# Optimization experiments

Hardware: AMD Instinct MI355X
Metric: run time of the kernel (lower is better)

## Reference

```python
import jax, jax.numpy as jnp
import numpy as np

N, IC, H, OC, E = 50000, 128, 128, 64, 800000
EPS = 1e-5


def _sage(x, src, dst, wl, wr, b):
    # PyG SAGEConv (mean aggr): out = lin_l(mean_j x_j) + lin_r(x)
    msg = x[src]                                    # [E, d] gather
    s = jax.ops.segment_sum(msg, dst, num_segments=N)
    cnt = jax.ops.segment_sum(jnp.ones((src.shape[0],), x.dtype), dst, num_segments=N)
    mean = s / jnp.clip(cnt, 1.0)[:, None]
    return mean @ wl.T + b + x @ wr.T


def _bn_relu(x, g, be):
    # training-mode BatchNorm1d over node axis (biased var), then ReLU
    m = jnp.mean(x, axis=0)
    v = jnp.mean((x - m) ** 2, axis=0)
    return jax.nn.relu((x - m) * jax.lax.rsqrt(v + EPS) * g + be)


def setup_inputs() -> dict:
    key = jax.random.key(0)
    ks = jax.random.split(key, 16)
    d = {
        "x": jax.random.normal(ks[0], (N, IC), jnp.float32),
        "ei": jax.random.randint(ks[1], (2, E), 0, N, jnp.int32),
        # SAGEConv 1..3: lin_l (with bias) on aggregated, lin_r (no bias) on root
        "w1l": jax.random.normal(ks[2], (H, IC), jnp.float32) / np.sqrt(IC),
        "w1r": jax.random.normal(ks[3], (H, IC), jnp.float32) / np.sqrt(IC),
        "b1c": jnp.zeros((H,), jnp.float32),
        "w2l": jax.random.normal(ks[4], (H, H), jnp.float32) / np.sqrt(H),
        "w2r": jax.random.normal(ks[5], (H, H), jnp.float32) / np.sqrt(H),
        "b2c": jnp.zeros((H,), jnp.float32),
        "w3l": jax.random.normal(ks[6], (H, H), jnp.float32) / np.sqrt(H),
        "w3r": jax.random.normal(ks[7], (H, H), jnp.float32) / np.sqrt(H),
        "b3c": jnp.zeros((H,), jnp.float32),
        # BatchNorm affine params
        "g1": jnp.ones((H,), jnp.float32), "be1": jnp.zeros((H,), jnp.float32),
        "g2": jnp.ones((H,), jnp.float32), "be2": jnp.zeros((H,), jnp.float32),
        "g3": jnp.ones((H,), jnp.float32), "be3": jnp.zeros((H,), jnp.float32),
        # head Linear
        "wh": jax.random.normal(ks[8], (OC, H), jnp.float32) / np.sqrt(H),
        "bh": jnp.zeros((OC,), jnp.float32),
    }
    return d


def reference(x, ei, w1l, w1r, b1c, w2l, w2r, b2c, w3l, w3r, b3c,
              g1, be1, g2, be2, g3, be3, wh, bh):
    src, dst = ei[0], ei[1]
    h = _bn_relu(_sage(x, src, dst, w1l, w1r, b1c), g1, be1)
    # dropout omitted (deterministic reference / eval semantics)
    h = _bn_relu(_sage(h, src, dst, w2l, w2r, b2c), g2, be2)
    h = _bn_relu(_sage(h, src, dst, w3l, w3r, b3c), g3, be3)
    return h @ wh.T + bh
```

## Files before the change

kernel.cpp:

```cpp
#include <hip/hip_runtime.h>

static constexpr int FC = 128;

typedef __attribute__((ext_vector_type(8))) __bf16 bf16x8;
typedef __attribute__((ext_vector_type(4))) float f32x4;

__device__ __forceinline__ unsigned short f2bf(float f) {
  unsigned u = __float_as_uint(f);
  unsigned r = (u + 0x7FFF + ((u >> 16) & 1)) >> 16;
  return (unsigned short)r;
}
__device__ __forceinline__ float bf2f(unsigned short h) {
  return __uint_as_float((unsigned)h << 16);
}
__device__ __forceinline__ unsigned pk_i8x4(int q0, int q1, int q2, int q3) {
  return (unsigned)(q0 & 0xff) | ((unsigned)(q1 & 0xff) << 8) |
         ((unsigned)(q2 & 0xff) << 16) | ((unsigned)(q3 & 0xff) << 24);
}

__global__ __launch_bounds__(256) void zero_kernel(int* __restrict__ deg,
                                                   float* __restrict__ stats, int n) {
  int i = blockIdx.x * 256 + threadIdx.x;
  if (i < n) deg[i] = 0;
  if (i < 768) stats[i] = 0.f;
}

__global__ __launch_bounds__(256) void convert_kernel(
    const float* __restrict__ x, const float* __restrict__ w1l, const float* __restrict__ w1r,
    const float* __restrict__ w2l, const float* __restrict__ w2r,
    const float* __restrict__ w3l, const float* __restrict__ w3r,
    const float* __restrict__ wh,
    unsigned short* __restrict__ x_bf, unsigned* __restrict__ xi8,
    float* __restrict__ xsc,
    unsigned short* __restrict__ wc1,
    unsigned short* __restrict__ wc2, unsigned short* __restrict__ wc3,
    unsigned short* __restrict__ whb, int n, int nxq) {
  int b = blockIdx.x;
  int t = threadIdx.x;
  if (b < nxq) {
    int row = b * 8 + (t >> 5);
    int lane = t & 31;
    if (row >= n) return;
    float4 a = *reinterpret_cast<const float4*>(x + (size_t)row * FC + lane * 4);
    ushort4 o = {f2bf(a.x), f2bf(a.y), f2bf(a.z), f2bf(a.w)};
    *reinterpret_cast<ushort4*>(x_bf + (size_t)row * FC + lane * 4) = o;
    float m = fmaxf(fmaxf(fabsf(a.x), fabsf(a.y)), fmaxf(fabsf(a.z), fabsf(a.w)));
    m = fmaxf(m, __shfl_xor(m, 1));
    m = fmaxf(m, __shfl_xor(m, 2));
    m = fmaxf(m, __shfl_xor(m, 4));
    m = fmaxf(m, __shfl_xor(m, 8));
    m = fmaxf(m, __shfl_xor(m, 16));
    float inv = 127.0f / fmaxf(m, 1e-30f);
    int q0 = (int)rintf(a.x * inv), q1 = (int)rintf(a.y * inv);
    int q2 = (int)rintf(a.z * inv), q3 = (int)rintf(a.w * inv);
    xi8[(size_t)row * 32 + lane] = pk_i8x4(q0, q1, q2, q3);
    if (lane == 0) xsc[row] = m * (1.0f / 127.0f);
    return;
  }
  int r = b - nxq;
  if (r < 48) {
    int layer = r >> 4;
    const float* wl = layer == 0 ? w1l : (layer == 1 ? w2l : w3l);
    const float* wr = layer == 0 ? w1r : (layer == 1 ? w2r : w3r);
    unsigned short* out = layer == 0 ? wc1 : (layer == 1 ? wc2 : wc3);
    int i = (r & 15) * 256 + t;
    int row = i >> 5;
    int k8 = (i & 31) * 8;
    const float* src = (k8 < 128) ? (wl + (size_t)row * 128 + k8)
                                  : (wr + (size_t)row * 128 + (k8 - 128));
    float4 a = *reinterpret_cast<const float4*>(src);
    float4 c = *reinterpret_cast<const float4*>(src + 4);
    ushort4 o0 = {f2bf(a.x), f2bf(a.y), f2bf(a.z), f2bf(a.w)};
    ushort4 o1 = {f2bf(c.x), f2bf(c.y), f2bf(c.z), f2bf(c.w)};
    unsigned short* q = out + (size_t)row * 256 + k8;
    *reinterpret_cast<ushort4*>(q) = o0;
    *reinterpret_cast<ushort4*>(q + 4) = o1;
  } else {
    int i = (r - 48) * 256 + t;
    const float* p = wh + (size_t)i * 8;
    float4 a = *reinterpret_cast<const float4*>(p);
    float4 c = *reinterpret_cast<const float4*>(p + 4);
    ushort4 o0 = {f2bf(a.x), f2bf(a.y), f2bf(a.z), f2bf(a.w)};
    ushort4 o1 = {f2bf(c.x), f2bf(c.y), f2bf(c.z), f2bf(c.w)};
    unsigned short* q = whb + (size_t)i * 8;
    *reinterpret_cast<ushort4*>(q) = o0;
    *reinterpret_cast<ushort4*>(q + 4) = o1;
  }
}

__global__ void count_kernel(const int* __restrict__ dst, int* __restrict__ deg,
                             int* __restrict__ rank, int e) {
  int i = blockIdx.x * blockDim.x + threadIdx.x;
  if (i < e) rank[i] = atomicAdd(&deg[dst[i]], 1);
}

__global__ __launch_bounds__(256) void scan1_kernel(const int* __restrict__ deg,
                                                    int* __restrict__ bsum, int n) {
  int i = blockIdx.x * 256 + threadIdx.x;
  int v = (i < n) ? deg[i] : 0;
  __shared__ int ls[256];
  ls[threadIdx.x] = v;
  __syncthreads();
  for (int d = 128; d > 0; d >>= 1) {
    if (threadIdx.x < (unsigned)d) ls[threadIdx.x] += ls[threadIdx.x + d];
    __syncthreads();
  }
  if (threadIdx.x == 0) bsum[blockIdx.x] = ls[0];
}

__global__ __launch_bounds__(256) void scan23_kernel(const int* __restrict__ deg,
                                                     const int* __restrict__ bsum,
                                                     int* __restrict__ off, int n, int nb) {
  __shared__ int bls[256];
  __shared__ int ls[256];
  int t = threadIdx.x;
  int bv = (t < nb) ? bsum[t] : 0;
  bls[t] = bv;
  __syncthreads();
  for (int d = 1; d < 256; d <<= 1) {
    int u = (t >= d) ? bls[t - d] : 0;
    __syncthreads();
    bls[t] += u;
    __syncthreads();
  }
  int i = blockIdx.x * 256 + t;
  int v = (i < n) ? deg[i] : 0;
  ls[t] = v;
  __syncthreads();
  for (int d = 1; d < 256; d <<= 1) {
    int u = (t >= d) ? ls[t - d] : 0;
    __syncthreads();
    ls[t] += u;
    __syncthreads();
  }
  int base = blockIdx.x ? bls[blockIdx.x - 1] : 0;
  if (i < n) off[i] = base + ls[t] - v;
  if (blockIdx.x == 0 && t == 0) off[n] = bls[nb - 1];
}

__global__ void fill_kernel(const int* __restrict__ src, const int* __restrict__ dst,
                            const int* __restrict__ rank, const int* __restrict__ off,
                            int* __restrict__ csr, int e) {
  int i = blockIdx.x * blockDim.x + threadIdx.x;
  if (i < e) csr[off[dst[i]] + rank[i]] = src[i];
}

template <bool BNIN>
__global__ __launch_bounds__(256) void aggregate_kernel(const unsigned* __restrict__ xi8,
                                                        const float* __restrict__ xsc,
                                                        const int* __restrict__ off,
                                                        const int* __restrict__ csr,
                                                        unsigned short* __restrict__ agg,
                                                        const float* __restrict__ stats,
                                                        const float* __restrict__ g,
                                                        const float* __restrict__ be,
                                                        float invn, int n) {
  int hw = (int)((blockIdx.x * blockDim.x + threadIdx.x) >> 5);
  int lane = threadIdx.x & 31;
  if (hw >= n) return;

  float sc0 = 1.f, sc1 = 1.f, sc2 = 1.f, sc3 = 1.f;
  float sh0 = 0.f, sh1 = 0.f, sh2 = 0.f, sh3 = 0.f;
  if (BNIN) {
    int c0 = lane * 4;
    float4 s  = *reinterpret_cast<const float4*>(stats + c0);
    float4 s2 = *reinterpret_cast<const float4*>(stats + 128 + c0);
    float4 gv = *reinterpret_cast<const float4*>(g + c0);
    float4 bv = *reinterpret_cast<const float4*>(be + c0);
    float m0 = s.x * invn, m1 = s.y * invn, m2 = s.z * invn, m3 = s.w * invn;
    sc0 = gv.x * rsqrtf(fmaxf(s2.x * invn - m0 * m0, 0.f) + 1e-5f);
    sc1 = gv.y * rsqrtf(fmaxf(s2.y * invn - m1 * m1, 0.f) + 1e-5f);
    sc2 = gv.z * rsqrtf(fmaxf(s2.z * invn - m2 * m2, 0.f) + 1e-5f);
    sc3 = gv.w * rsqrtf(fmaxf(s2.w * invn - m3 * m3, 0.f) + 1e-5f);
    sh0 = bv.x - m0 * sc0; sh1 = bv.y - m1 * sc1;
    sh2 = bv.z - m2 * sc2; sh3 = bv.w - m3 * sc3;
  }

  int s0 = off[hw], s1 = off[hw + 1];
  float a0 = 0.f, a1 = 0.f, a2 = 0.f, a3 = 0.f;

#define ACCV(u, sv)                                               \
  {                                                               \
    float q0 = (float)(((int)(u) << 24) >> 24);                   \
    float q1 = (float)(((int)(u) << 16) >> 24);                   \
    float q2 = (float)(((int)(u) << 8) >> 24);                    \
    float q3 = (float)((int)(u) >> 24);                           \
    if (BNIN) {                                                   \
      a0 += fmaxf(fmaf(q0, (sv) * sc0, sh0), 0.f);                \
      a1 += fmaxf(fmaf(q1, (sv) * sc1, sh1), 0.f);                \
      a2 += fmaxf(fmaf(q2, (sv) * sc2, sh2), 0.f);                \
      a3 += fmaxf(fmaf(q3, (sv) * sc3, sh3), 0.f);                \
    } else {                                                      \
      a0 = fmaf(q0, (sv), a0);                                    \
      a1 = fmaf(q1, (sv), a1);                                    \
      a2 = fmaf(q2, (sv), a2);                                    \
      a3 = fmaf(q3, (sv), a3);                                    \
    }                                                             \
  }

  int j = s0;
  for (; j + 8 <= s1; j += 8) {
    int i0 = csr[j],     i1 = csr[j + 1], i2 = csr[j + 2], i3 = csr[j + 3];
    int i4 = csr[j + 4], i5 = csr[j + 5], i6 = csr[j + 6], i7 = csr[j + 7];
    unsigned u0 = xi8[(size_t)i0 * 32 + lane];
    unsigned u1 = xi8[(size_t)i1 * 32 + lane];
    unsigned u2 = xi8[(size_t)i2 * 32 + lane];
    unsigned u3 = xi8[(size_t)i3 * 32 + lane];
    unsigned u4 = xi8[(size_t)i4 * 32 + lane];
    unsigned u5 = xi8[(size_t)i5 * 32 + lane];
    unsigned u6 = xi8[(size_t)i6 * 32 + lane];
    unsigned u7 = xi8[(size_t)i7 * 32 + lane];
    float sv0 = xsc[i0], sv1 = xsc[i1], sv2 = xsc[i2], sv3 = xsc[i3];
    float sv4 = xsc[i4], sv5 = xsc[i5], sv6 = xsc[i6], sv7 = xsc[i7];
    ACCV(u0, sv0) ACCV(u1, sv1) ACCV(u2, sv2) ACCV(u3, sv3)
    ACCV(u4, sv4) ACCV(u5, sv5) ACCV(u6, sv6) ACCV(u7, sv7)
  }
  for (; j < s1; j++) {
    int i0 = csr[j];
    unsigned u0 = xi8[(size_t)i0 * 32 + lane];
    float sv0 = xsc[i0];
    ACCV(u0, sv0)
  }
#undef ACCV

  int d = s1 - s0;
  float inv = 1.0f / (float)(d > 0 ? d : 1);
  ushort4 o = {f2bf(a0 * inv), f2bf(a1 * inv), f2bf(a2 * inv), f2bf(a3 * inv)};
  *reinterpret_cast<ushort4*>(agg + (size_t)hw * FC + lane * 4) = o;
}

template <int NCOLS, int KTOT, bool DUAL, bool OUT_BF, bool STATS, bool BNIN, bool OUT_I8>
__global__ __launch_bounds__(256) void gemm_kernel(const unsigned short* __restrict__ A1,
                                                   const unsigned short* __restrict__ A2,
                                                   const unsigned short* __restrict__ W,
                                                   const float* __restrict__ bias,
                                                   void* __restrict__ Cout,
                                                   unsigned char* __restrict__ h8,
                                                   float* __restrict__ hsc,
                                                   float* __restrict__ statsOut,
                                                   const float* __restrict__ statsIn,
                                                   const float* __restrict__ g,
                                                   const float* __restrict__ be,
                                                   float invn, int nrows) {
  constexpr int NKT = KTOT / 32;
  constexpr int NCF = NCOLS / 16;
  constexpr int RB = KTOT * 2;
  constexpr int WBYTES = NCOLS * KTOT * 2;
  __shared__ __align__(16) unsigned char Wl[WBYTES];
  __shared__ float scv[128], shv[128];

  int t = threadIdx.x;

  {
    constexpr int CH = WBYTES / 16 / 256;
#pragma unroll
    for (int c = 0; c < CH; c++) {
      int byte = (c * 256 + t) * 16;
      int row = byte / RB;
      int cb = byte % RB;
      float4 v = *reinterpret_cast<const float4*>(reinterpret_cast<const char*>(W) + byte);
      *reinterpret_cast<float4*>(Wl + row * RB + (cb ^ ((row & 7) << 4))) = v;
    }
  }

  if (BNIN && t < 128) {
    float mean = statsIn[t] * invn;
    float var = fmaxf(statsIn[128 + t] * invn - mean * mean, 0.f);
    float s = g[t] * rsqrtf(var + 1e-5f);
    scv[t] = s;
    shv[t] = be[t] - mean * s;
  }

  int w = t >> 6;
  int l = t & 63;
  int lm = l & 15;
  int hi = l >> 4;
  int lk = hi * 8;
  int row = blockIdx.x * 64 + w * 16 + lm;
  int rclamp = min(row, nrows - 1);

  bf16x8 a[NKT];
#pragma unroll
  for (int kt = 0; kt < NKT; kt++) {
    const unsigned short* Ap;
    int kk;
    if (!DUAL || kt < NKT / 2) { Ap = A1; kk = kt * 32; }
    else                       { Ap = A2; kk = (kt - NKT / 2) * 32; }
    a[kt] = *reinterpret_cast<const bf16x8*>(Ap + (size_t)rclamp * 128 + kk + lk);
  }

  f32x4 acc[NCF];
#pragma unroll
  for (int cf = 0; cf < NCF; cf++) acc[cf] = {0.f, 0.f, 0.f, 0.f};

  __syncthreads();

  if (BNIN) {
#pragma unroll
    for (int kt = 0; kt < NKT; kt++) {
      if (!DUAL || kt >= NKT / 2) {
        int ch0 = (DUAL ? (kt - NKT / 2) : kt) * 32 + lk;
#pragma unroll
        for (int j = 0; j < 8; j++) {
          float v = (float)a[kt][j];
          v = fmaxf(fmaf(v, scv[ch0 + j], shv[ch0 + j]), 0.f);
          a[kt][j] = (__bf16)v;
        }
      }
    }
  }

#pragma unroll
  for (int kt = 0; kt < NKT; kt++) {
#pragma unroll
    for (int cf = 0; cf < NCF; cf++) {
      int r = cf * 16 + lm;
      int cb = kt * 64 + hi * 16;
      bf16x8 b = *reinterpret_cast<const bf16x8*>(Wl + r * RB + (cb ^ ((r & 7) << 4)));
      acc[cf] = __builtin_amdgcn_mfma_f32_16x16x32_bf16(a[kt], b, acc[cf], 0, 0, 0);
    }
  }

#pragma unroll
  for (int cf = 0; cf < NCF; cf++) {
    float bs = bias[cf * 16 + lm];
#pragma unroll
    for (int r = 0; r < 4; r++) acc[cf][r] += bs;
  }

  float qinv[4], qs[4];
  if (OUT_I8) {
#pragma unroll
    for (int r = 0; r < 4; r++) {
      float m = 0.f;
#pragma unroll
      for (int cf = 0; cf < NCF; cf++) m = fmaxf(m, fabsf(acc[cf][r]));
      m = fmaxf(m, __shfl_xor(m, 1));
      m = fmaxf(m, __shfl_xor(m, 2));
      m = fmaxf(m, __shfl_xor(m, 4));
      m = fmaxf(m, __shfl_xor(m, 8));
      qinv[r] = 127.0f / fmaxf(m, 1e-30f);
      qs[r] = m * (1.0f / 127.0f);
    }
  }

  __shared__ float wsum[4][NCOLS];
  __shared__ float wsq[4][NCOLS];

  int orow0 = blockIdx.x * 64 + w * 16 + hi * 4;
#pragma unroll
  for (int cf = 0; cf < NCF; cf++) {
    int col = cf * 16 + lm;
    float s = 0.f, s2 = 0.f;
#pragma unroll
    for (int r = 0; r < 4; r++) {
      int orow = orow0 + r;
      bool ok = orow < nrows;
      float v = acc[cf][r];
      if (ok) {
        if (OUT_BF)
          ((unsigned short*)Cout)[(size_t)orow * NCOLS + col] = f2bf(v);
        else
          ((float*)Cout)[(size_t)orow * NCOLS + col] = v;
        if (OUT_I8)
          h8[(size_t)orow * NCOLS + col] = (unsigned char)((int)rintf(v * qinv[r]) & 0xff);
      }
      if (STATS) {
        float vv = ok ? v : 0.f;
        s += vv; s2 += vv * vv;
      }
    }
    if (STATS) {
      s  += __shfl_xor(s, 16);  s  += __shfl_xor(s, 32);
      s2 += __shfl_xor(s2, 16); s2 += __shfl_xor(s2, 32);
      if (l < 16) { wsum[w][col] = s; wsq[w][col] = s2; }
    }
  }
  if (OUT_I8 && lm == 0) {
#pragma unroll
    for (int r = 0; r < 4; r++) {
      int orow = orow0 + r;
      if (orow < nrows) hsc[orow] = qs[r];
    }
  }
  if (STATS) {
    __syncthreads();
    if (t < NCOLS) {
      atomicAdd(&statsOut[t], wsum[0][t] + wsum[1][t] + wsum[2][t] + wsum[3][t]);
    } else if (t < 2 * NCOLS) {
      int c = t - NCOLS;
      atomicAdd(&statsOut[t], wsq[0][c] + wsq[1][c] + wsq[2][c] + wsq[3][c]);
    }
  }
}

extern "C" void kernel_launch(void* const* d_in, const int* in_sizes, int n_in,
                              void* d_out, int out_size, void* d_ws, size_t ws_size,
                              hipStream_t stream) {
  const float* x   = (const float*)d_in[0];
  const int*   ei  = (const int*)d_in[1];
  const float* w1l = (const float*)d_in[2];
  const float* w1r = (const float*)d_in[3];
  const float* b1c = (const float*)d_in[4];
  const float* w2l = (const float*)d_in[5];
  const float* w2r = (const float*)d_in[6];
  const float* b2c = (const float*)d_in[7];
  const float* w3l = (const float*)d_in[8];
  const float* w3r = (const float*)d_in[9];
  const float* b3c = (const float*)d_in[10];
  const float* g1  = (const float*)d_in[11];
  const float* be1 = (const float*)d_in[12];
  const float* g2  = (const float*)d_in[13];
  const float* be2 = (const float*)d_in[14];
  const float* g3  = (const float*)d_in[15];
  const float* be3 = (const float*)d_in[16];
  const float* wh  = (const float*)d_in[17];
  const float* bh  = (const float*)d_in[18];

  int n = in_sizes[0] / FC;
  int e = in_sizes[1] / 2;
  const int* srcI = ei;
  const int* dstI = ei + e;

  char* p = (char*)d_ws;
  auto take = [&](size_t bytes) {
    char* q = p;
    p += (bytes + 255) & ~(size_t)255;
    return q;
  };
  int nb = (n + 255) / 256;
  int* deg  = (int*)take((size_t)n * 4);
  int* off  = (int*)take((size_t)(n + 1) * 4);
  int* bsum = (int*)take((size_t)nb * 4);
  int* rank = (int*)take((size_t)e * 4);
  int* csr  = (int*)take((size_t)e * 4);
  unsigned short* x_bf = (unsigned short*)take((size_t)n * FC * 2);
  unsigned short* agg  = (unsigned short*)take((size_t)n * FC * 2);
  unsigned short* h1   = (unsigned short*)take((size_t)n * FC * 2);
  unsigned short* h2   = (unsigned short*)take((size_t)n * FC * 2);
  unsigned char*  ai8  = (unsigned char*)take((size_t)n * FC);
  float*          asc  = (float*)take((size_t)n * 4);
  unsigned short* wc1  = (unsigned short*)take(128 * 256 * 2);
  unsigned short* wc2  = (unsigned short*)take(128 * 256 * 2);
  unsigned short* wc3  = (unsigned short*)take(128 * 256 * 2);
  unsigned short* whb  = (unsigned short*)take(64 * 128 * 2);
  float* stats = (float*)take(3 * 256 * 4);

  float invn = 1.0f / (float)n;
  int nxq = (n + 7) / 8;

  zero_kernel<<<nb, 256, 0, stream>>>(deg, stats, n);
  convert_kernel<<<nxq + 52, 256, 0, stream>>>(x, w1l, w1r, w2l, w2r, w3l, w3r, wh,
                                               x_bf, (unsigned*)ai8, asc,
                                               wc1, wc2, wc3, whb, n, nxq);

  count_kernel<<<(e + 255) / 256, 256, 0, stream>>>(dstI, deg, rank, e);
  scan1_kernel<<<nb, 256, 0, stream>>>(deg, bsum, n);
  scan23_kernel<<<nb, 256, 0, stream>>>(deg, bsum, off, n, nb);
  fill_kernel<<<(e + 255) / 256, 256, 0, stream>>>(srcI, dstI, rank, off, csr, e);

  int gb = (n + 63) / 64;
  int ab = (n + 7) / 8;

  aggregate_kernel<false><<<ab, 256, 0, stream>>>((const unsigned*)ai8, asc, off, csr, agg,
                                                  nullptr, nullptr, nullptr, invn, n);
  gemm_kernel<128, 256, true, true, true, false, true><<<gb, 256, 0, stream>>>(
      agg, x_bf, wc1, b1c, h1, ai8, asc, stats, nullptr, nullptr, nullptr, invn, n);

  aggregate_kernel<true><<<ab, 256, 0, stream>>>((const unsigned*)ai8, asc, off, csr, agg,
                                                 stats, g1, be1, invn, n);
  gemm_kernel<128, 256, true, true, true, true, true><<<gb, 256, 0, stream>>>(
      agg, h1, wc2, b2c, h2, ai8, asc, stats + 256, stats, g1, be1, invn, n);

  aggregate_kernel<true><<<ab, 256, 0, stream>>>((const unsigned*)ai8, asc, off, csr, agg,
                                                 stats + 256, g2, be2, invn, n);
  gemm_kernel<128, 256, true, true, true, true, false><<<gb, 256, 0, stream>>>(
      agg, h2, wc3, b3c, h1, nullptr, nullptr, stats + 512, stats + 256, g2, be2, invn, n);

  gemm_kernel<64, 128, false, false, false, true, false><<<gb, 256, 0, stream>>>(
      h1, nullptr, whb, bh, d_out, nullptr, nullptr, nullptr, stats + 512, g3, be3, invn, n);
}
```

Baseline: 261.7 us.

## Split int8 feature table into two column halves and aggregate each half separately

The int8 quantized node features are stored as two separate 64-column tables, and each aggregation is split into two launches, one per half, using 16 lanes per node. Each half table is 3.2 MB instead of 6.4 MB, so the random neighbor gathers should hit in cache more often. CSR index reads become nontemporal loads. The cost is that the CSR indices and scales are read twice and there are extra kernel launches.

Measured after the change: 313.1 us. +19.7%, slower.

```diff
diff --git a/kernel.cpp b/kernel.cpp
--- a/kernel.cpp
+++ b/kernel.cpp
@@ -30,7 +30,7 @@
     const float* __restrict__ w2l, const float* __restrict__ w2r,
     const float* __restrict__ w3l, const float* __restrict__ w3r,
     const float* __restrict__ wh,
-    unsigned short* __restrict__ x_bf, unsigned* __restrict__ xi8,
+    unsigned short* __restrict__ x_bf, unsigned* __restrict__ ta, unsigned* __restrict__ tb,
     float* __restrict__ xsc,
     unsigned short* __restrict__ wc1,
     unsigned short* __restrict__ wc2, unsigned short* __restrict__ wc3,
@@ -53,7 +53,9 @@
     float inv = 127.0f / fmaxf(m, 1e-30f);
     int q0 = (int)rintf(a.x * inv), q1 = (int)rintf(a.y * inv);
     int q2 = (int)rintf(a.z * inv), q3 = (int)rintf(a.w * inv);
-    xi8[(size_t)row * 32 + lane] = pk_i8x4(q0, q1, q2, q3);
+    unsigned u = pk_i8x4(q0, q1, q2, q3);
+    if (lane < 16) ta[(size_t)row * 16 + lane] = u;
+    else           tb[(size_t)row * 16 + (lane - 16)] = u;
     if (lane == 0) xsc[row] = m * (1.0f / 127.0f);
     return;
   }
@@ -145,8 +147,8 @@
   if (i < e) csr[off[dst[i]] + rank[i]] = src[i];
 }
 
-template <bool BNIN>
-__global__ __launch_bounds__(256) void aggregate_kernel(const unsigned* __restrict__ xi8,
+template <int HALF, bool BNIN>
+__global__ __launch_bounds__(256) void aggregate_kernel(const unsigned* __restrict__ tab,
                                                         const float* __restrict__ xsc,
                                                         const int* __restrict__ off,
                                                         const int* __restrict__ csr,
@@ -155,14 +157,14 @@
                                                         const float* __restrict__ g,
                                                         const float* __restrict__ be,
                                                         float invn, int n) {
-  int hw = (int)((blockIdx.x * blockDim.x + threadIdx.x) >> 5);
-  int lane = threadIdx.x & 31;
-  if (hw >= n) return;
+  int node = (int)((blockIdx.x * blockDim.x + threadIdx.x) >> 4);
+  int lane = threadIdx.x & 15;
+  if (node >= n) return;
 
   float sc0 = 1.f, sc1 = 1.f, sc2 = 1.f, sc3 = 1.f;
   float sh0 = 0.f, sh1 = 0.f, sh2 = 0.f, sh3 = 0.f;
   if (BNIN) {
-    int c0 = lane * 4;
+    int c0 = HALF * 64 + lane * 4;
     float4 s  = *reinterpret_cast<const float4*>(stats + c0);
     float4 s2 = *reinterpret_cast<const float4*>(stats + 128 + c0);
     float4 gv = *reinterpret_cast<const float4*>(g + c0);
@@ -176,7 +178,7 @@
     sh2 = bv.z - m2 * sc2; sh3 = bv.w - m3 * sc3;
   }
 
-  int s0 = off[hw], s1 = off[hw + 1];
+  int s0 = off[node], s1 = off[node + 1];
   float a0 = 0.f, a1 = 0.f, a2 = 0.f, a3 = 0.f;
 
 #define ACCV(u, sv)                                               \
@@ -200,24 +202,30 @@
 
   int j = s0;
   for (; j + 8 <= s1; j += 8) {
-    int i0 = csr[j],     i1 = csr[j + 1], i2 = csr[j + 2], i3 = csr[j + 3];
-    int i4 = csr[j + 4], i5 = csr[j + 5], i6 = csr[j + 6], i7 = csr[j + 7];
-    unsigned u0 = xi8[(size_t)i0 * 32 + lane];
-    unsigned u1 = xi8[(size_t)i1 * 32 + lane];
-    unsigned u2 = xi8[(size_t)i2 * 32 + lane];
-    unsigned u3 = xi8[(size_t)i3 * 32 + lane];
-    unsigned u4 = xi8[(size_t)i4 * 32 + lane];
-    unsigned u5 = xi8[(size_t)i5 * 32 + lane];
-    unsigned u6 = xi8[(size_t)i6 * 32 + lane];
-    unsigned u7 = xi8[(size_t)i7 * 32 + lane];
+    int i0 = __builtin_nontemporal_load(csr + j);
+    int i1 = __builtin_nontemporal_load(csr + j + 1);
+    int i2 = __builtin_nontemporal_load(csr + j + 2);
+    int i3 = __builtin_nontemporal_load(csr + j + 3);
+    int i4 = __builtin_nontemporal_load(csr + j + 4);
+    int i5 = __builtin_nontemporal_load(csr + j + 5);
+    int i6 = __builtin_nontemporal_load(csr + j + 6);
+    int i7 = __builtin_nontemporal_load(csr + j + 7);
+    unsigned u0 = tab[(size_t)i0 * 16 + lane];
+    unsigned u1 = tab[(size_t)i1 * 16 + lane];
+    unsigned u2 = tab[(size_t)i2 * 16 + lane];
+    unsigned u3 = tab[(size_t)i3 * 16 + lane];
+    unsigned u4 = tab[(size_t)i4 * 16 + lane];
+    unsigned u5 = tab[(size_t)i5 * 16 + lane];
+    unsigned u6 = tab[(size_t)i6 * 16 + lane];
+    unsigned u7 = tab[(size_t)i7 * 16 + lane];
     float sv0 = xsc[i0], sv1 = xsc[i1], sv2 = xsc[i2], sv3 = xsc[i3];
     float sv4 = xsc[i4], sv5 = xsc[i5], sv6 = xsc[i6], sv7 = xsc[i7];
     ACCV(u0, sv0) ACCV(u1, sv1) ACCV(u2, sv2) ACCV(u3, sv3)
     ACCV(u4, sv4) ACCV(u5, sv5) ACCV(u6, sv6) ACCV(u7, sv7)
   }
   for (; j < s1; j++) {
-    int i0 = csr[j];
-    unsigned u0 = xi8[(size_t)i0 * 32 + lane];
+    int i0 = __builtin_nontemporal_load(csr + j);
+    unsigned u0 = tab[(size_t)i0 * 16 + lane];
     float sv0 = xsc[i0];
     ACCV(u0, sv0)
   }
@@ -226,7 +234,7 @@
   int d = s1 - s0;
   float inv = 1.0f / (float)(d > 0 ? d : 1);
   ushort4 o = {f2bf(a0 * inv), f2bf(a1 * inv), f2bf(a2 * inv), f2bf(a3 * inv)};
-  *reinterpret_cast<ushort4*>(agg + (size_t)hw * FC + lane * 4) = o;
+  *reinterpret_cast<ushort4*>(agg + (size_t)node * FC + HALF * 64 + lane * 4) = o;
 }
 
 template <int NCOLS, int KTOT, bool DUAL, bool OUT_BF, bool STATS, bool BNIN, bool OUT_I8>
@@ -235,7 +243,8 @@
                                                    const unsigned short* __restrict__ W,
                                                    const float* __restrict__ bias,
                                                    void* __restrict__ Cout,
-                                                   unsigned char* __restrict__ h8,
+                                                   unsigned char* __restrict__ i8a,
+                                                   unsigned char* __restrict__ i8b,
                                                    float* __restrict__ hsc,
                                                    float* __restrict__ statsOut,
                                                    const float* __restrict__ statsIn,
@@ -362,8 +371,11 @@
           ((unsigned short*)Cout)[(size_t)orow * NCOLS + col] = f2bf(v);
         else
           ((float*)Cout)[(size_t)orow * NCOLS + col] = v;
-        if (OUT_I8)
-          h8[(size_t)orow * NCOLS + col] = (unsigned char)((int)rintf(v * qinv[r]) & 0xff);
+        if (OUT_I8) {
+          unsigned char qb = (unsigned char)((int)rintf(v * qinv[r]) & 0xff);
+          if (col < 64) i8a[(size_t)orow * 64 + col] = qb;
+          else          i8b[(size_t)orow * 64 + (col - 64)] = qb;
+        }
       }
       if (STATS) {
         float vv = ok ? v : 0.f;
@@ -438,7 +450,8 @@
   unsigned short* agg  = (unsigned short*)take((size_t)n * FC * 2);
   unsigned short* h1   = (unsigned short*)take((size_t)n * FC * 2);
   unsigned short* h2   = (unsigned short*)take((size_t)n * FC * 2);
-  unsigned char*  ai8  = (unsigned char*)take((size_t)n * FC);
+  unsigned char*  i8a  = (unsigned char*)take((size_t)n * 64);
+  unsigned char*  i8b  = (unsigned char*)take((size_t)n * 64);
   float*          asc  = (float*)take((size_t)n * 4);
   unsigned short* wc1  = (unsigned short*)take(128 * 256 * 2);
   unsigned short* wc2  = (unsigned short*)take(128 * 256 * 2);
@@ -451,7 +464,7 @@
 
   zero_kernel<<<nb, 256, 0, stream>>>(deg, stats, n);
   convert_kernel<<<nxq + 52, 256, 0, stream>>>(x, w1l, w1r, w2l, w2r, w3l, w3r, wh,
-                                               x_bf, (unsigned*)ai8, asc,
+                                               x_bf, (unsigned*)i8a, (unsigned*)i8b, asc,
                                                wc1, wc2, wc3, whb, n, nxq);
 
   count_kernel<<<(e + 255) / 256, 256, 0, stream>>>(dstI, deg, rank, e);
@@ -460,23 +473,31 @@
   fill_kernel<<<(e + 255) / 256, 256, 0, stream>>>(srcI, dstI, rank, off, csr, e);
 
   int gb = (n + 63) / 64;
-  int ab = (n + 7) / 8;
-
-  aggregate_kernel<false><<<ab, 256, 0, stream>>>((const unsigned*)ai8, asc, off, csr, agg,
-                                                  nullptr, nullptr, nullptr, invn, n);
+  int qb = (n + 15) / 16;
+
+  aggregate_kernel<0, false><<<qb, 256, 0, stream>>>((const unsigned*)i8a, asc, off, csr, agg,
+                                                     nullptr, nullptr, nullptr, invn, n);
+  aggregate_kernel<1, false><<<qb, 256, 0, stream>>>((const unsigned*)i8b, asc, off, csr, agg,
+                                                     nullptr, nullptr, nullptr, invn, n);
   gemm_kernel<128, 256, true, true, true, false, true><<<gb, 256, 0, stream>>>(
-      agg, x_bf, wc1, b1c, h1, ai8, asc, stats, nullptr, nullptr, nullptr, invn, n);
-
-  aggregate_kernel<true><<<ab, 256, 0, stream>>>((const unsigned*)ai8, asc, off, csr, agg,
-                                                 stats, g1, be1, invn, n);
+      agg, x_bf, wc1, b1c, h1, i8a, i8b, asc, stats, nullptr, nullptr, nullptr, invn, n);
+
+  aggregate_kernel<0, true><<<qb, 256, 0, stream>>>((const unsigned*)i8a, asc, off, csr, agg,
+                                                    stats, g1, be1, invn, n);
+  aggregate_kernel<1, true><<<qb, 256, 0, stream>>>((const unsigned*)i8b, asc, off, csr, agg,
+                                                    stats, g1, be1, invn, n);
   gemm_kernel<128, 256, true, true, true, true, true><<<gb, 256, 0, stream>>>(
-      agg, h1, wc2, b2c, h2, ai8, asc, stats + 256, stats, g1, be1, invn, n);
-
-  aggregate_kernel<true><<<ab, 256, 0, stream>>>((const unsigned*)ai8, asc, off, csr, agg,
-                                                 stats + 256, g2, be2, invn, n);
+      agg, h1, wc2, b2c, h2, i8a, i8b, asc, stats + 256, stats, g1, be1, invn, n);
+
+  aggregate_kernel<0, true><<<qb, 256, 0, stream>>>((const unsigned*)i8a, asc, off, csr, agg,
+                                                    stats + 256, g2, be2, invn, n);
+  aggregate_kernel<1, true><<<qb, 256, 0, stream>>>((const unsigned*)i8b, asc, off, csr, agg,
+                                                    stats + 256, g2, be2, invn, n);
   gemm_kernel<128, 256, true, true, true, true, false><<<gb, 256, 0, stream>>>(
-      agg, h2, wc3, b3c, h1, nullptr, nullptr, stats + 512, stats + 256, g2, be2, invn, n);
+      agg, h2, wc3, b3c, h1, nullptr, nullptr, nullptr, stats + 512, stats + 256, g2, be2,
+      invn, n);
 
   gemm_kernel<64, 128, false, false, false, true, false><<<gb, 256, 0, stream>>>(
-      h1, nullptr, whb, bh, d_out, nullptr, nullptr, nullptr, stats + 512, g3, be3, invn, n);
-}
+      h1, nullptr, whb, bh, d_out, nullptr, nullptr, nullptr, nullptr, stats + 512, g3, be3,
+      invn, n);
+}
```

## Switch int8 gather table from per-row scales to a single global tensor scale

Applied to the files above, without the earlier changes.

Replaces the per-row int8 quantization scale with one global absmax per tensor. The absmax is collected through atomicMax in the producer kernels, and separate quant kernels write the int8 table. This removes the per-neighbour scale gather and multiply in the aggregate loop, and folds the count kernel into the conversion kernel. It adds three extra quant passes over bf16 activations, and a global scale loses precision for rows with small magnitudes.

Measured after the change: 424.8 us. +62.4%, slower.

```diff
diff --git a/kernel.cpp b/kernel.cpp
--- a/kernel.cpp
+++ b/kernel.cpp
@@ -19,45 +19,57 @@
 }
 
 __global__ __launch_bounds__(256) void zero_kernel(int* __restrict__ deg,
-                                                   float* __restrict__ stats, int n) {
+                                                   float* __restrict__ stats,
+                                                   unsigned* __restrict__ smax, int n) {
   int i = blockIdx.x * 256 + threadIdx.x;
   if (i < n) deg[i] = 0;
   if (i < 768) stats[i] = 0.f;
-}
-
-__global__ __launch_bounds__(256) void convert_kernel(
+  if (i < 4) smax[i] = 0u;
+}
+
+__global__ __launch_bounds__(256) void pre_kernel(
+    const int* __restrict__ dst, int* __restrict__ deg, int* __restrict__ rank, int e,
     const float* __restrict__ x, const float* __restrict__ w1l, const float* __restrict__ w1r,
     const float* __restrict__ w2l, const float* __restrict__ w2r,
     const float* __restrict__ w3l, const float* __restrict__ w3r,
     const float* __restrict__ wh,
-    unsigned short* __restrict__ x_bf, unsigned* __restrict__ xi8,
-    float* __restrict__ xsc,
+    unsigned short* __restrict__ x_bf, unsigned* __restrict__ smax,
     unsigned short* __restrict__ wc1,
     unsigned short* __restrict__ wc2, unsigned short* __restrict__ wc3,
-    unsigned short* __restrict__ whb, int n, int nxq) {
+    unsigned short* __restrict__ whb, int nx8, int cb, int xb) {
   int b = blockIdx.x;
   int t = threadIdx.x;
-  if (b < nxq) {
-    int row = b * 8 + (t >> 5);
-    int lane = t & 31;
-    if (row >= n) return;
-    float4 a = *reinterpret_cast<const float4*>(x + (size_t)row * FC + lane * 4);
-    ushort4 o = {f2bf(a.x), f2bf(a.y), f2bf(a.z), f2bf(a.w)};
-    *reinterpret_cast<ushort4*>(x_bf + (size_t)row * FC + lane * 4) = o;
-    float m = fmaxf(fmaxf(fabsf(a.x), fabsf(a.y)), fmaxf(fabsf(a.z), fabsf(a.w)));
+  if (b < cb) {
+    int i = b * 256 + t;
+    if (i < e) rank[i] = atomicAdd(&deg[dst[i]], 1);
+    return;
+  }
+  int r = b - cb;
+  if (r < xb) {
+    int i = r * 256 + t;
+    float m = 0.f;
+    if (i < nx8) {
+      const float* p = x + (size_t)i * 8;
+      float4 a = *reinterpret_cast<const float4*>(p);
+      float4 c = *reinterpret_cast<const float4*>(p + 4);
+      ushort4 o0 = {f2bf(a.x), f2bf(a.y), f2bf(a.z), f2bf(a.w)};
+      ushort4 o1 = {f2bf(c.x), f2bf(c.y), f2bf(c.z), f2bf(c.w)};
+      unsigned short* q = x_bf + (size_t)i * 8;
+      *reinterpret_cast<ushort4*>(q) = o0;
+      *reinterpret_cast<ushort4*>(q + 4) = o1;
+      m = fmaxf(fmaxf(fmaxf(fabsf(a.x), fabsf(a.y)), fmaxf(fabsf(a.z), fabsf(a.w))),
+                fmaxf(fmaxf(fabsf(c.x), fabsf(c.y)), fmaxf(fabsf(c.z), fabsf(c.w))));
+    }
     m = fmaxf(m, __shfl_xor(m, 1));
     m = fmaxf(m, __shfl_xor(m, 2));
     m = fmaxf(m, __shfl_xor(m, 4));
     m = fmaxf(m, __shfl_xor(m, 8));
     m = fmaxf(m, __shfl_xor(m, 16));
-    float inv = 127.0f / fmaxf(m, 1e-30f);
-    int q0 = (int)rintf(a.x * inv), q1 = (int)rintf(a.y * inv);
-    int q2 = (int)rintf(a.z * inv), q3 = (int)rintf(a.w * inv);
-    xi8[(size_t)row * 32 + lane] = pk_i8x4(q0, q1, q2, q3);
-    if (lane == 0) xsc[row] = m * (1.0f / 127.0f);
+    m = fmaxf(m, __shfl_xor(m, 32));
+    if ((t & 63) == 0) atomicMax(&smax[0], __float_as_uint(m));
     return;
   }
-  int r = b - nxq;
+  r -= xb;
   if (r < 48) {
     int layer = r >> 4;
     const float* wl = layer == 0 ? w1l : (layer == 1 ? w2l : w3l);
@@ -88,10 +100,22 @@
   }
 }
 
-__global__ void count_kernel(const int* __restrict__ dst, int* __restrict__ deg,
-                             int* __restrict__ rank, int e) {
-  int i = blockIdx.x * blockDim.x + threadIdx.x;
-  if (i < e) rank[i] = atomicAdd(&deg[dst[i]], 1);
+__global__ __launch_bounds__(256) void quant_kernel(const unsigned short* __restrict__ hbf,
+                                                    const unsigned* __restrict__ smax,
+                                                    unsigned* __restrict__ tab, int n16) {
+  int i = blockIdx.x * 256 + threadIdx.x;
+  if (i >= n16) return;
+  float mx = __uint_as_float(*smax);
+  float qi = 127.0f / fmaxf(mx, 1e-30f);
+  const unsigned short* p = hbf + (size_t)i * 8;
+  ushort4 v0 = *reinterpret_cast<const ushort4*>(p);
+  ushort4 v1 = *reinterpret_cast<const ushort4*>(p + 4);
+  int q0 = (int)rintf(bf2f(v0.x) * qi), q1 = (int)rintf(bf2f(v0.y) * qi);
+  int q2 = (int)rintf(bf2f(v0.z) * qi), q3 = (int)rintf(bf2f(v0.w) * qi);
+  int q4 = (int)rintf(bf2f(v1.x) * qi), q5 = (int)rintf(bf2f(v1.y) * qi);
+  int q6 = (int)rintf(bf2f(v1.z) * qi), q7 = (int)rintf(bf2f(v1.w) * qi);
+  uint2 u = {pk_i8x4(q0, q1, q2, q3), pk_i8x4(q4, q5, q6, q7)};
+  *reinterpret_cast<uint2*>(tab + (size_t)i * 2) = u;
 }
 
 __global__ __launch_bounds__(256) void scan1_kernel(const int* __restrict__ deg,
@@ -146,8 +170,8 @@
 }
 
 template <bool BNIN>
-__global__ __launch_bounds__(256) void aggregate_kernel(const unsigned* __restrict__ xi8,
-                                                        const float* __restrict__ xsc,
+__global__ __launch_bounds__(256) void aggregate_kernel(const unsigned* __restrict__ tab,
+                                                        const unsigned* __restrict__ smax,
                                                         const int* __restrict__ off,
                                                         const int* __restrict__ csr,
                                                         unsigned short* __restrict__ agg,
@@ -159,7 +183,9 @@
   int lane = threadIdx.x & 31;
   if (hw >= n) return;
 
-  float sc0 = 1.f, sc1 = 1.f, sc2 = 1.f, sc3 = 1.f;
+  float sdeq = __uint_as_float(*smax) * (1.0f / 127.0f);
+
+  float sc0 = sdeq, sc1 = sdeq, sc2 = sdeq, sc3 = sdeq;
   float sh0 = 0.f, sh1 = 0.f, sh2 = 0.f, sh3 = 0.f;
   if (BNIN) {
     int c0 = lane * 4;
@@ -168,33 +194,31 @@
     float4 gv = *reinterpret_cast<const float4*>(g + c0);
     float4 bv = *reinterpret_cast<const float4*>(be + c0);
     float m0 = s.x * invn, m1 = s.y * invn, m2 = s.z * invn, m3 = s.w * invn;
-    sc0 = gv.x * rsqrtf(fmaxf(s2.x * invn - m0 * m0, 0.f) + 1e-5f);
-    sc1 = gv.y * rsqrtf(fmaxf(s2.y * invn - m1 * m1, 0.f) + 1e-5f);
-    sc2 = gv.z * rsqrtf(fmaxf(s2.z * invn - m2 * m2, 0.f) + 1e-5f);
-    sc3 = gv.w * rsqrtf(fmaxf(s2.w * invn - m3 * m3, 0.f) + 1e-5f);
-    sh0 = bv.x - m0 * sc0; sh1 = bv.y - m1 * sc1;
-    sh2 = bv.z - m2 * sc2; sh3 = bv.w - m3 * sc3;
+    float b0 = gv.x * rsqrtf(fmaxf(s2.x * invn - m0 * m0, 0.f) + 1e-5f);
+    float b1 = gv.y * rsqrtf(fmaxf(s2.y * invn - m1 * m1, 0.f) + 1e-5f);
+    float b2 = gv.z * rsqrtf(fmaxf(s2.z * invn - m2 * m2, 0.f) + 1e-5f);
+    float b3 = gv.w * rsqrtf(fmaxf(s2.w * invn - m3 * m3, 0.f) + 1e-5f);
+    sh0 = bv.x - m0 * b0; sh1 = bv.y - m1 * b1;
+    sh2 = bv.z - m2 * b2; sh3 = bv.w - m3 * b3;
+    sc0 = b0 * sdeq; sc1 = b1 * sdeq; sc2 = b2 * sdeq; sc3 = b3 * sdeq;
   }
 
   int s0 = off[hw], s1 = off[hw + 1];
   float a0 = 0.f, a1 = 0.f, a2 = 0.f, a3 = 0.f;
 
-#define ACCV(u, sv)                                               \
+#define ACCV(u)                                                   \
   {                                                               \
     float q0 = (float)(((int)(u) << 24) >> 24);                   \
     float q1 = (float)(((int)(u) << 16) >> 24);                   \
     float q2 = (float)(((int)(u) << 8) >> 24);                    \
     float q3 = (float)((int)(u) >> 24);                           \
     if (BNIN) {                                                   \
-      a0 += fmaxf(fmaf(q0, (sv) * sc0, sh0), 0.f);                \
-      a1 += fmaxf(fmaf(q1, (sv) * sc1, sh1), 0.f);                \
-      a2 += fmaxf(fmaf(q2, (sv) * sc2, sh2), 0.f);                \
-      a3 += fmaxf(fmaf(q3, (sv) * sc3, sh3), 0.f);                \
+      a0 += fmaxf(fmaf(q0, sc0, sh0), 0.f);                       \
+      a1 += fmaxf(fmaf(q1, sc1, sh1), 0.f);                       \
+      a2 += fmaxf(fmaf(q2, sc2, sh2), 0.f);                       \
+      a3 += fmaxf(fmaf(q3, sc3, sh3), 0.f);                       \
     } else {                                                      \
-      a0 = fmaf(q0, (sv), a0);                                    \
-      a1 = fmaf(q1, (sv), a1);                                    \
-      a2 = fmaf(q2, (sv), a2);                                    \
-      a3 = fmaf(q3, (sv), a3);                                    \
+      a0 += q0; a1 += q1; a2 += q2; a3 += q3;                     \
     }                                                             \
   }
 
@@ -202,41 +226,36 @@
   for (; j + 8 <= s1; j += 8) {
     int i0 = csr[j],     i1 = csr[j + 1], i2 = csr[j + 2], i3 = csr[j + 3];
     int i4 = csr[j + 4], i5 = csr[j + 5], i6 = csr[j + 6], i7 = csr[j + 7];
-    unsigned u0 = xi8[(size_t)i0 * 32 + lane];
-    unsigned u1 = xi8[(size_t)i1 * 32 + lane];
-    unsigned u2 = xi8[(size_t)i2 * 32 + lane];
-    unsigned u3 = xi8[(size_t)i3 * 32 + lane];
-    unsigned u4 = xi8[(size_t)i4 * 32 + lane];
-    unsigned u5 = xi8[(size_t)i5 * 32 + lane];
-    unsigned u6 = xi8[(size_t)i6 * 32 + lane];
-    unsigned u7 = xi8[(size_t)i7 * 32 + lane];
-    float sv0 = xsc[i0], sv1 = xsc[i1], sv2 = xsc[i2], sv3 = xsc[i3];
-    float sv4 = xsc[i4], sv5 = xsc[i5], sv6 = xsc[i6], sv7 = xsc[i7];
-    ACCV(u0, sv0) ACCV(u1, sv1) ACCV(u2, sv2) ACCV(u3, sv3)
-    ACCV(u4, sv4) ACCV(u5, sv5) ACCV(u6, sv6) ACCV(u7, sv7)
+    unsigned u0 = tab[(size_t)i0 * 32 + lane];
+    unsigned u1 = tab[(size_t)i1 * 32 + lane];
+    unsigned u2 = tab[(size_t)i2 * 32 + lane];
+    unsigned u3 = tab[(size_t)i3 * 32 + lane];
+    unsigned u4 = tab[(size_t)i4 * 32 + lane];
+    unsigned u5 = tab[(size_t)i5 * 32 + lane];
+    unsigned u6 = tab[(size_t)i6 * 32 + lane];
+    unsigned u7 = tab[(size_t)i7 * 32 + lane];
+    ACCV(u0) ACCV(u1) ACCV(u2) ACCV(u3) ACCV(u4) ACCV(u5) ACCV(u6) ACCV(u7)
   }
   for (; j < s1; j++) {
-    int i0 = csr[j];
-    unsigned u0 = xi8[(size_t)i0 * 32 + lane];
-    float sv0 = xsc[i0];
-    ACCV(u0, sv0)
+    unsigned u0 = tab[(size_t)csr[j] * 32 + lane];
+    ACCV(u0)
   }
 #undef ACCV
 
   int d = s1 - s0;
   float inv = 1.0f / (float)(d > 0 ? d : 1);
+  if (!BNIN) inv *= sdeq;
   ushort4 o = {f2bf(a0 * inv), f2bf(a1 * inv), f2bf(a2 * inv), f2bf(a3 * inv)};
   *reinterpret_cast<ushort4*>(agg + (size_t)hw * FC + lane * 4) = o;
 }
 
-template <int NCOLS, int KTOT, bool DUAL, bool OUT_BF, bool STATS, bool BNIN, bool OUT_I8>
+template <int NCOLS, int KTOT, bool DUAL, bool OUT_BF, bool STATS, bool BNIN, bool SMAX>
 __global__ __launch_bounds__(256) void gemm_kernel(const unsigned short* __restrict__ A1,
                                                    const unsigned short* __restrict__ A2,
                                                    const unsigned short* __restrict__ W,
                                                    const float* __restrict__ bias,
                                                    void* __restrict__ Cout,
-                                                   unsigned char* __restrict__ h8,
-                                                   float* __restrict__ hsc,
+                                                   unsigned* __restrict__ smaxOut,
                                                    float* __restrict__ statsOut,
                                                    const float* __restrict__ statsIn,
                                                    const float* __restrict__ g,
@@ -328,20 +347,19 @@
     for (int r = 0; r < 4; r++) acc[cf][r] += bs;
   }
 
-  float qinv[4], qs[4];
-  if (OUT_I8) {
-#pragma unroll
-    for (int r = 0; r < 4; r++) {
-      float m = 0.f;
-#pragma unroll
-      for (int cf = 0; cf < NCF; cf++) m = fmaxf(m, fabsf(acc[cf][r]));
-      m = fmaxf(m, __shfl_xor(m, 1));
-      m = fmaxf(m, __shfl_xor(m, 2));
-      m = fmaxf(m, __shfl_xor(m, 4));
-      m = fmaxf(m, __shfl_xor(m, 8));
-      qinv[r] = 127.0f / fmaxf(m, 1e-30f);
-      qs[r] = m * (1.0f / 127.0f);
-    }
+  if (SMAX) {
+    float m = 0.f;
+#pragma unroll
+    for (int cf = 0; cf < NCF; cf++)
+#pragma unroll
+      for (int r = 0; r < 4; r++) m = fmaxf(m, fabsf(acc[cf][r]));
+    m = fmaxf(m, __shfl_xor(m, 1));
+    m = fmaxf(m, __shfl_xor(m, 2));
+    m = fmaxf(m, __shfl_xor(m, 4));
+    m = fmaxf(m, __shfl_xor(m, 8));
+    m = fmaxf(m, __shfl_xor(m, 16));
+    m = fmaxf(m, __shfl_xor(m, 32));
+    if (l == 0) atomicMax(smaxOut, __float_as_uint(m));
   }
 
   __shared__ float wsum[4][NCOLS];
@@ -362,8 +380,6 @@
           ((unsigned short*)Cout)[(size_t)orow * NCOLS + col] = f2bf(v);
         else
           ((float*)Cout)[(size_t)orow * NCOLS + col] = v;
-        if (OUT_I8)
-          h8[(size_t)orow * NCOLS + col] = (unsigned char)((int)rintf(v * qinv[r]) & 0xff);
       }
       if (STATS) {
         float vv = ok ? v : 0.f;
@@ -374,13 +390,6 @@
       s  += __shfl_xor(s, 16);  s  += __shfl_xor(s, 32);
       s2 += __shfl_xor(s2, 16); s2 += __shfl_xor(s2, 32);
       if (l < 16) { wsum[w][col] = s; wsq[w][col] = s2; }
-    }
-  }
-  if (OUT_I8 && lm == 0) {
-#pragma unroll
-    for (int r = 0; r < 4; r++) {
-      int orow = orow0 + r;
-      if (orow < nrows) hsc[orow] = qs[r];
     }
   }
   if (STATS) {
@@ -439,44 +448,48 @@
   unsigned short* h1   = (unsigned short*)take((size_t)n * FC * 2);
   unsigned short* h2   = (unsigned short*)take((size_t)n * FC * 2);
   unsigned char*  ai8  = (unsigned char*)take((size_t)n * FC);
-  float*          asc  = (float*)take((size_t)n * 4);
   unsigned short* wc1  = (unsigned short*)take(128 * 256 * 2);
   unsigned short* wc2  = (unsigned short*)take(128 * 256 * 2);
   unsigned short* wc3  = (unsigned short*)take(128 * 256 * 2);
   unsigned short* whb  = (unsigned short*)take(64 * 128 * 2);
-  float* stats = (float*)take(3 * 256 * 4);
+  float*    stats = (float*)take(3 * 256 * 4);
+  unsigned* smax  = (unsigned*)take(4 * 4);
 
   float invn = 1.0f / (float)n;
-  int nxq = (n + 7) / 8;
-
-  zero_kernel<<<nb, 256, 0, stream>>>(deg, stats, n);
-  convert_kernel<<<nxq + 52, 256, 0, stream>>>(x, w1l, w1r, w2l, w2r, w3l, w3r, wh,
-                                               x_bf, (unsigned*)ai8, asc,
-                                               wc1, wc2, wc3, whb, n, nxq);
-
-  count_kernel<<<(e + 255) / 256, 256, 0, stream>>>(dstI, deg, rank, e);
+  int nx8 = n * 16;
+  int cb = (e + 255) / 256;
+  int xb = (nx8 + 255) / 256;
+
+  zero_kernel<<<nb, 256, 0, stream>>>(deg, stats, smax, n);
+  pre_kernel<<<cb + xb + 52, 256, 0, stream>>>(dstI, deg, rank, e,
+                                               x, w1l, w1r, w2l, w2r, w3l, w3r, wh,
+                                               x_bf, smax, wc1, wc2, wc3, whb, nx8, cb, xb);
+
   scan1_kernel<<<nb, 256, 0, stream>>>(deg, bsum, n);
   scan23_kernel<<<nb, 256, 0, stream>>>(deg, bsum, off, n, nb);
-  fill_kernel<<<(e + 255) / 256, 256, 0, stream>>>(srcI, dstI, rank, off, csr, e);
+  fill_kernel<<<cb, 256, 0, stream>>>(srcI, dstI, rank, off, csr, e);
+  quant_kernel<<<xb, 256, 0, stream>>>(x_bf, smax, (unsigned*)ai8, nx8);
 
   int gb = (n + 63) / 64;
   int ab = (n + 7) / 8;
 
-  aggregate_kernel<false><<<ab, 256, 0, stream>>>((const unsigned*)ai8, asc, off, csr, agg,
+  aggregate_kernel<false><<<ab, 256, 0, stream>>>((const unsigned*)ai8, smax, off, csr, agg,
                                                   nullptr, nullptr, nullptr, invn, n);
   gemm_kernel<128, 256, true, true, true, false, true><<<gb, 256, 0, stream>>>(
-      agg, x_bf, wc1, b1c, h1, ai8, asc, stats, nullptr, nullptr, nullptr, invn, n);
-
-  aggregate_kernel<true><<<ab, 256, 0, stream>>>((const unsigned*)ai8, asc, off, csr, agg,
+      agg, x_bf, wc1, b1c, h1, smax + 1, stats, nullptr, nullptr, nullptr, invn, n);
+  quant_kernel<<<xb, 256, 0, stream>>>(h1, smax + 1, (unsigned*)ai8, nx8);
+
+  aggregate_kernel<true><<<ab, 256, 0, stream>>>((const unsigned*)ai8, smax + 1, off, csr, agg,
                                                  stats, g1, be1, invn, n);
   gemm_kernel<128, 256, true, true, true, true, true><<<gb, 256, 0, stream>>>(
-      agg, h1, wc2, b2c, h2, ai8, asc, stats + 256, stats, g1, be1, invn, n);
-
-  aggregate_kernel<true><<<ab, 256, 0, stream>>>((const unsigned*)ai8, asc, off, csr, agg,
+      agg, h1, wc2, b2c, h2, smax + 2, stats + 256, stats, g1, be1, invn, n);
+  quant_kernel<<<xb, 256, 0, stream>>>(h2, smax + 2, (unsigned*)ai8, nx8);
+
+  aggregate_kernel<true><<<ab, 256, 0, stream>>>((const unsigned*)ai8, smax + 2, off, csr, agg,
                                                  stats + 256, g2, be2, invn, n);
   gemm_kernel<128, 256, true, true, true, true, false><<<gb, 256, 0, stream>>>(
-      agg, h2, wc3, b3c, h1, nullptr, nullptr, stats + 512, stats + 256, g2, be2, invn, n);
+      agg, h2, wc3, b3c, h1, nullptr, stats + 512, stats + 256, g2, be2, invn, n);
 
   gemm_kernel<64, 128, false, false, false, true, false><<<gb, 256, 0, stream>>>(
-      h1, nullptr, whb, bh, d_out, nullptr, nullptr, nullptr, stats + 512, g3, be3, invn, n);
-}
+      h1, nullptr, whb, bh, d_out, nullptr, nullptr, stats + 512, g3, be3, invn, n);
+}
```

## Replace global atomic degree count with per-block LDS histograms and merge

Applied to the files above, without the earlier changes.

Degree counting for CSR construction moves from per-edge global atomics into 64 blocks. Each block builds a packed 16-bit-pair histogram of destination counts in shared memory (25000 words, 100KB), and a merge kernel computes per-block base offsets and degrees. The fill kernel then adds the per-block base to the local rank. This removes contended global atomics but runs the histogram on only 64 blocks and adds a merge kernel that reads and writes 64×n entries. ghist and base reuse the agg and h1 buffers, and 100KB of LDS per block limits occupancy.

Measured after the change: 268.6 us. 2.6% more time.

```diff
diff --git a/kernel.cpp b/kernel.cpp
--- a/kernel.cpp
+++ b/kernel.cpp
@@ -1,6 +1,7 @@
 #include <hip/hip_runtime.h>
 
 static constexpr int FC = 128;
+static constexpr int HB = 64;
 
 typedef __attribute__((ext_vector_type(8))) __bf16 bf16x8;
 typedef __attribute__((ext_vector_type(4))) float f32x4;
@@ -18,10 +19,8 @@
          ((unsigned)(q2 & 0xff) << 16) | ((unsigned)(q3 & 0xff) << 24);
 }
 
-__global__ __launch_bounds__(256) void zero_kernel(int* __restrict__ deg,
-                                                   float* __restrict__ stats, int n) {
+__global__ __launch_bounds__(256) void zero_kernel(float* __restrict__ stats) {
   int i = blockIdx.x * 256 + threadIdx.x;
-  if (i < n) deg[i] = 0;
   if (i < 768) stats[i] = 0.f;
 }
 
@@ -88,10 +87,46 @@
   }
 }
 
-__global__ void count_kernel(const int* __restrict__ dst, int* __restrict__ deg,
-                             int* __restrict__ rank, int e) {
-  int i = blockIdx.x * blockDim.x + threadIdx.x;
-  if (i < e) rank[i] = atomicAdd(&deg[dst[i]], 1);
+__global__ __launch_bounds__(256) void hist_kernel(const int* __restrict__ dst,
+                                                   unsigned* __restrict__ ghist,
+                                                   unsigned short* __restrict__ lrank,
+                                                   int e, int chunk, int nw) {
+  __shared__ unsigned hist[25000];
+  int b = blockIdx.x;
+  int t = threadIdx.x;
+  for (int w = t; w < nw; w += 256) hist[w] = 0u;
+  __syncthreads();
+  int i0 = b * chunk;
+  int i1 = min(i0 + chunk, e);
+  for (int i = i0 + t; i < i1; i += 256) {
+    int d = dst[i];
+    int w = d >> 1;
+    int sh = (d & 1) << 4;
+    unsigned old = atomicAdd(&hist[w], 1u << sh);
+    lrank[i] = (unsigned short)((old >> sh) & 0xffffu);
+  }
+  __syncthreads();
+  unsigned* gh = ghist + (size_t)b * nw;
+  for (int w = t; w < nw; w += 256) gh[w] = hist[w];
+}
+
+__global__ __launch_bounds__(256) void merge_kernel(const unsigned* __restrict__ ghist,
+                                                    unsigned* __restrict__ base,
+                                                    int* __restrict__ deg, int n, int nw) {
+  int w = blockIdx.x * 256 + threadIdx.x;
+  if (w >= nw) return;
+  int n0 = 2 * w, n1 = 2 * w + 1;
+  unsigned c0 = 0, c1 = 0;
+  for (int b = 0; b < HB; b++) {
+    unsigned u = ghist[(size_t)b * nw + w];
+    unsigned* bp = base + (size_t)b * n;
+    bp[n0] = c0;
+    if (n1 < n) bp[n1] = c1;
+    c0 += u & 0xffffu;
+    c1 += u >> 16;
+  }
+  deg[n0] = (int)c0;
+  if (n1 < n) deg[n1] = (int)c1;
 }
 
 __global__ __launch_bounds__(256) void scan1_kernel(const int* __restrict__ deg,
@@ -139,10 +174,14 @@
 }
 
 __global__ void fill_kernel(const int* __restrict__ src, const int* __restrict__ dst,
-                            const int* __restrict__ rank, const int* __restrict__ off,
-                            int* __restrict__ csr, int e) {
+                            const unsigned short* __restrict__ lrank,
+                            const int* __restrict__ off, const unsigned* __restrict__ base,
+                            int* __restrict__ csr, int e, int chunk, int n) {
   int i = blockIdx.x * blockDim.x + threadIdx.x;
-  if (i < e) csr[off[dst[i]] + rank[i]] = src[i];
+  if (i >= e) return;
+  int b = i / chunk;
+  int d = dst[i];
+  csr[off[d] + (int)base[(size_t)b * n + d] + (int)lrank[i]] = src[i];
 }
 
 template <bool BNIN>
@@ -429,10 +468,17 @@
     return q;
   };
   int nb = (n + 255) / 256;
+  int nw = (n + 1) / 2;
+  int chunk = (e + HB - 1) / HB;
+  int nxq = (n + 7) / 8;
+  int gb = (n + 63) / 64;
+  int ab = (n + 7) / 8;
+  int cb = (e + 255) / 256;
+
   int* deg  = (int*)take((size_t)n * 4);
   int* off  = (int*)take((size_t)(n + 1) * 4);
   int* bsum = (int*)take((size_t)nb * 4);
-  int* rank = (int*)take((size_t)e * 4);
+  unsigned short* lrank = (unsigned short*)take((size_t)e * 2);
   int* csr  = (int*)take((size_t)e * 4);
   unsigned short* x_bf = (unsigned short*)take((size_t)n * FC * 2);
   unsigned short* agg  = (unsigned short*)take((size_t)n * FC * 2);
@@ -446,21 +492,21 @@
   unsigned short* whb  = (unsigned short*)take(64 * 128 * 2);
   float* stats = (float*)take(3 * 256 * 4);
 
+  unsigned* ghist = (unsigned*)agg;
+  unsigned* base  = (unsigned*)h1;
+
   float invn = 1.0f / (float)n;
-  int nxq = (n + 7) / 8;
-
-  zero_kernel<<<nb, 256, 0, stream>>>(deg, stats, n);
+
+  zero_kernel<<<3, 256, 0, stream>>>(stats);
   convert_kernel<<<nxq + 52, 256, 0, stream>>>(x, w1l, w1r, w2l, w2r, w3l, w3r, wh,
                                                x_bf, (unsigned*)ai8, asc,
                                                wc1, wc2, wc3, whb, n, nxq);
 
-  count_kernel<<<(e + 255) / 256, 256, 0, stream>>>(dstI, deg, rank, e);
+  hist_kernel<<<HB, 256, 0, stream>>>(dstI, ghist, lrank, e, chunk, nw);
+  merge_kernel<<<(nw + 255) / 256, 256, 0, stream>>>(ghist, base, deg, n, nw);
   scan1_kernel<<<nb, 256, 0, stream>>>(deg, bsum, n);
   scan23_kernel<<<nb, 256, 0, stream>>>(deg, bsum, off, n, nb);
-  fill_kernel<<<(e + 255) / 256, 256, 0, stream>>>(srcI, dstI, rank, off, csr, e);
-
-  int gb = (n + 63) / 64;
-  int ab = (n + 7) / 8;
+  fill_kernel<<<cb, 256, 0, stream>>>(srcI, dstI, lrank, off, base, csr, e, chunk, n);
 
   aggregate_kernel<false><<<ab, 256, 0, stream>>>((const unsigned*)ai8, asc, off, csr, agg,
                                                   nullptr, nullptr, nullptr, invn, n);
```
